# Kernel tuning notes

Measured on AMD Instinct MI355X. Metric: run time of the kernel, lower is better.

The kernel has to match this reference:

```python
import jax, jax.numpy as jnp
import numpy as np

H = 356  # CHAR_EMBED_DIM (100) + ELMO_EMBED_DIM (256)
CHAR_VOCAB = 96
CHAR_DIM = 100
N_FILT = 100
KW = 5
N_CTX = 8192
N_Q = 1024
W_CHARS = 16


def setup_inputs() -> dict:
    key = jax.random.key(0)
    ks = iter(jax.random.split(key, 32))
    s = 0.05
    inp = {}
    inp['ctx_char_ids'] = jax.random.randint(next(ks), (N_CTX, W_CHARS), 0, CHAR_VOCAB, dtype=jnp.int32)
    inp['q_char_ids'] = jax.random.randint(next(ks), (N_Q, W_CHARS), 0, CHAR_VOCAB, dtype=jnp.int32)
    inp['ctx_elmo'] = jax.random.normal(next(ks), (N_CTX, 256), jnp.float32)
    inp['q_elmo'] = jax.random.normal(next(ks), (N_Q, 256), jnp.float32)
    inp['char_emb'] = jax.random.normal(next(ks), (CHAR_VOCAB, CHAR_DIM), jnp.float32)
    inp['conv_w'] = jax.random.normal(next(ks), (N_FILT, CHAR_DIM, KW), jnp.float32) * s
    inp['conv_b'] = jax.random.normal(next(ks), (N_FILT,), jnp.float32) * s
    # Highway: 2 layers of plain + gate Linear(356 -> 356)
    inp['hw_pw'] = jax.random.normal(next(ks), (2, H, H), jnp.float32) * s
    inp['hw_pb'] = jax.random.normal(next(ks), (2, H), jnp.float32) * s
    inp['hw_gw'] = jax.random.normal(next(ks), (2, H, H), jnp.float32) * s
    inp['hw_gb'] = jax.random.normal(next(ks), (2, H), jnp.float32) * s
    # BiLSTM layer 0: input 356; layer 1: input 712. dims: [dir, 4H, Din]
    inp['w_ih0'] = jax.random.normal(next(ks), (2, 4 * H, H), jnp.float32) * s
    inp['w_hh0'] = jax.random.normal(next(ks), (2, 4 * H, H), jnp.float32) * s
    inp['b_ih0'] = jax.random.normal(next(ks), (2, 4 * H), jnp.float32) * s
    inp['b_hh0'] = jax.random.normal(next(ks), (2, 4 * H), jnp.float32) * s
    inp['w_ih1'] = jax.random.normal(next(ks), (2, 4 * H, 2 * H), jnp.float32) * s
    inp['w_hh1'] = jax.random.normal(next(ks), (2, 4 * H, H), jnp.float32) * s
    inp['b_ih1'] = jax.random.normal(next(ks), (2, 4 * H), jnp.float32) * s
    inp['b_hh1'] = jax.random.normal(next(ks), (2, 4 * H), jnp.float32) * s
    # randomize_init_hidden=True: random (h0, c0), shared per original code.
    h0 = jax.random.normal(next(ks), (2, 2, H), jnp.float32)  # [layer, dir, H]
    inp['h0'] = h0
    inp['c0'] = h0  # original returns (init_hidden, init_hidden)
    return inp


def _highway(x, pw, pb, gw, gb):
    for i in range(2):
        g = jax.nn.sigmoid(x @ gw[i].T + gb[i])
        p = jax.nn.relu(x @ pw[i].T + pb[i])
        x = g * p + (1.0 - g) * x
    return x


def _lstm_dir(x, w_ih, w_hh, b_ih, b_hh, h0, c0):
    # x: [T, Din]; PyTorch gate order i, f, g, o
    xg = x @ w_ih.T + (b_ih + b_hh)  # [T, 4H]

    def step(carry, xg_t):
        h, c = carry
        gates = xg_t + h @ w_hh.T
        i, f, g, o = jnp.split(gates, 4)
        i = jax.nn.sigmoid(i)
        f = jax.nn.sigmoid(f)
        g = jnp.tanh(g)
        o = jax.nn.sigmoid(o)
        c = f * c + i * g
        h = o * jnp.tanh(c)
        return (h, c), h

    _, hs = jax.lax.scan(step, (h0, c0), xg)
    return hs  # [T, H]


def _bilstm_layer(x, w_ih, w_hh, b_ih, b_hh, h0, c0):
    fwd = _lstm_dir(x, w_ih[0], w_hh[0], b_ih[0], b_hh[0], h0[0], c0[0])
    bwd = _lstm_dir(x[::-1], w_ih[1], w_hh[1], b_ih[1], b_hh[1], h0[1], c0[1])[::-1]
    return jnp.concatenate([fwd, bwd], axis=-1)  # [T, 2H]


def _embed_doc(char_ids, elmo, char_emb, conv_w, conv_b, hw_pw, hw_pb, hw_gw, hw_gb,
               w_ih0, w_hh0, b_ih0, b_hh0, w_ih1, w_hh1, b_ih1, b_hh1, h0, c0):
    ce = char_emb[char_ids]                  # [N, W, 100]
    x = jnp.transpose(ce, (0, 2, 1))         # [N, 100, W]
    conv = jax.lax.conv_general_dilated(
        x, conv_w, window_strides=(1,), padding=[(KW // 2, KW // 2)],
        dimension_numbers=('NCH', 'OIH', 'NCH')) + conv_b[None, :, None]
    cnn_feat = conv.max(axis=2)              # [N, 100] maxpool over char positions
    feats = jnp.concatenate([cnn_feat, elmo], axis=1)  # [N, 356]
    hwy = _highway(feats, hw_pw, hw_pb, hw_gw, hw_gb)
    l1 = _bilstm_layer(hwy, w_ih0, w_hh0, b_ih0, b_hh0, h0[0], c0[0])
    l2 = _bilstm_layer(l1, w_ih1, w_hh1, b_ih1, b_hh1, h0[1], c0[1])
    return l2  # [N, 712]


def reference(ctx_char_ids, q_char_ids, ctx_elmo, q_elmo, char_emb, conv_w, conv_b,
              hw_pw, hw_pb, hw_gw, hw_gb,
              w_ih0, w_hh0, b_ih0, b_hh0, w_ih1, w_hh1, b_ih1, b_hh1, h0, c0):
    params = (char_emb, conv_w, conv_b, hw_pw, hw_pb, hw_gw, hw_gb,
              w_ih0, w_hh0, b_ih0, b_hh0, w_ih1, w_hh1, b_ih1, b_hh1, h0, c0)
    ctx_out = _embed_doc(ctx_char_ids, ctx_elmo, *params)
    q_out = _embed_doc(q_char_ids, q_elmo, *params)
    return (ctx_out, q_out)
```

## Files before the change

kernel.cpp:

```cpp
#include <hip/hip_runtime.h>
#include <hip/hip_bf16.h>

#define H_DIM 356
#define G4 1424
#define NCTX 8192
#define NQ 1024
#define NTOT 9216
#define CDIM 100
#define NFILT 100
#define KW 5
#define WCH 16

typedef _Float16 f16_t;

__device__ __forceinline__ float sigmoidf_fast(float x) {
    return 1.0f / (1.0f + __expf(-x));
}
__device__ __forceinline__ float tanhf_fast(float x) {
    return 2.0f / (1.0f + __expf(-2.0f * x)) - 1.0f;
}
__device__ __forceinline__ unsigned pack_f16x2(float a, float b) {
    _Float16 ha = (_Float16)a, hb = (_Float16)b;
    unsigned short ua = __builtin_bit_cast(unsigned short, ha);
    unsigned short ub = __builtin_bit_cast(unsigned short, hb);
    return (unsigned)ua | ((unsigned)ub << 16);
}
__device__ __forceinline__ unsigned short f16_bits(float a) {
    _Float16 ha = (_Float16)a;
    return __builtin_bit_cast(unsigned short, ha);
}

#define FDOT_S(ACC, W, HS) \
    asm("v_dot2_f32_f16 %0, %1, %2, %0" : "+v"(ACC) : "v"(W), "s"(HS))

__global__ __launch_bounds__(128) void cnn_highway_kernel(
    const int* __restrict__ ctx_ids, const int* __restrict__ q_ids,
    const float* __restrict__ ctx_elmo, const float* __restrict__ q_elmo,
    const float* __restrict__ char_emb, const float* __restrict__ conv_w,
    const float* __restrict__ conv_b,
    const float* __restrict__ hw_pw, const float* __restrict__ hw_pb,
    const float* __restrict__ hw_gw, const float* __restrict__ hw_gb,
    float* __restrict__ feats_out)
{
    __shared__ float s_ce[WCH][CDIM];
    __shared__ float s_feats[16][H_DIM];
    const int tid  = threadIdx.x;
    const int row0 = blockIdx.x * 16;

    for (int rr = 0; rr < 16; ++rr) {
        const int row = row0 + rr;
        const int* ids = (row < NCTX) ? (ctx_ids + (size_t)row * WCH)
                                      : (q_ids + (size_t)(row - NCTX) * WCH);
        for (int idx = tid; idx < WCH * CDIM; idx += 128) {
            int w = idx / CDIM, c = idx - w * CDIM;
            s_ce[w][c] = char_emb[(size_t)ids[w] * CDIM + c];
        }
        __syncthreads();
        if (tid < NFILT) {
            const int f = tid;
            float s[WCH];
            float bias = conv_b[f];
            #pragma unroll
            for (int p = 0; p < WCH; ++p) s[p] = bias;
            const float* wrow = conv_w + (size_t)f * CDIM * KW;
            for (int c0 = 0; c0 < CDIM; c0 += 4) {
                float wv[20];
                const float4* wp4 = (const float4*)(wrow + c0 * KW);
                #pragma unroll
                for (int u = 0; u < 5; ++u) {
                    float4 v = wp4[u];
                    wv[u * 4 + 0] = v.x; wv[u * 4 + 1] = v.y;
                    wv[u * 4 + 2] = v.z; wv[u * 4 + 3] = v.w;
                }
                #pragma unroll
                for (int cc = 0; cc < 4; ++cc) {
                    float ce[WCH];
                    #pragma unroll
                    for (int w = 0; w < WCH; ++w) ce[w] = s_ce[w][c0 + cc];
                    #pragma unroll
                    for (int p = 0; p < WCH; ++p) {
                        #pragma unroll
                        for (int k = 0; k < KW; ++k) {
                            const int wpos = p + k - 2;
                            if (wpos >= 0 && wpos < WCH)
                                s[p] = fmaf(ce[wpos], wv[cc * 5 + k], s[p]);
                        }
                    }
                }
            }
            float m = s[0];
            #pragma unroll
            for (int p = 1; p < WCH; ++p) m = fmaxf(m, s[p]);
            s_feats[rr][f] = m;
        }
        __syncthreads();
    }

    for (int idx = tid; idx < 16 * 256; idx += 128) {
        int rr = idx >> 8, c = idx & 255;
        int row = row0 + rr;
        float v = (row < NCTX) ? ctx_elmo[(size_t)row * 256 + c]
                               : q_elmo[(size_t)(row - NCTX) * 256 + c];
        s_feats[rr][CDIM + c] = v;
    }
    __syncthreads();

    for (int l = 0; l < 2; ++l) {
        float newv[3][16];
        for (int it = 0; it < 3; ++it) {
            const int j = it * 128 + tid;
            if (j < H_DIM) {
                float accP[16], accG[16];
                #pragma unroll
                for (int r = 0; r < 16; ++r) { accP[r] = 0.0f; accG[r] = 0.0f; }
                const float* pw = hw_pw + ((size_t)l * H_DIM + j) * H_DIM;
                const float* gw = hw_gw + ((size_t)l * H_DIM + j) * H_DIM;
                for (int k0 = 0; k0 < H_DIM; k0 += 4) {
                    float4 wpv4 = *(const float4*)(pw + k0);
                    float4 wgv4 = *(const float4*)(gw + k0);
                    float wp[4] = {wpv4.x, wpv4.y, wpv4.z, wpv4.w};
                    float wg[4] = {wgv4.x, wgv4.y, wgv4.z, wgv4.w};
                    #pragma unroll
                    for (int kk = 0; kk < 4; ++kk) {
                        #pragma unroll
                        for (int r = 0; r < 16; ++r) {
                            float fv = s_feats[r][k0 + kk];
                            accP[r] = fmaf(fv, wp[kk], accP[r]);
                            accG[r] = fmaf(fv, wg[kk], accG[r]);
                        }
                    }
                }
                const float pb = hw_pb[l * H_DIM + j];
                const float gb = hw_gb[l * H_DIM + j];
                #pragma unroll
                for (int r = 0; r < 16; ++r) {
                    float p = accP[r] + pb; p = p > 0.0f ? p : 0.0f;
                    float g = sigmoidf_fast(accG[r] + gb);
                    newv[it][r] = g * p + (1.0f - g) * s_feats[r][j];
                }
            }
        }
        __syncthreads();
        for (int it = 0; it < 3; ++it) {
            const int j = it * 128 + tid;
            if (j < H_DIM) {
                #pragma unroll
                for (int r = 0; r < 16; ++r) s_feats[r][j] = newv[it][r];
            }
        }
        __syncthreads();
    }

    for (int idx = tid; idx < 16 * H_DIM; idx += 128) {
        int rr = idx / H_DIM, j = idx - rr * H_DIM;
        feats_out[(size_t)(row0 + rr) * H_DIM + j] = s_feats[rr][j];
    }
}

__global__ __launch_bounds__(256) void gemm_nt_bias_kernel(
    const float* __restrict__ A, const float* __restrict__ B,
    const float* __restrict__ bia, const float* __restrict__ bib,
    f16_t* __restrict__ C, int M, int N, int K)
{
    const int z = blockIdx.z;
    const float* Bz = B + (size_t)z * N * K;
    f16_t* Cz = C + (size_t)z * M * N;
    const int n0 = blockIdx.x * 64;
    const int m0 = blockIdx.y * 64;
    __shared__ float As[64][17];
    __shared__ float Bs[64][17];
    const int tid = threadIdx.x;
    const int tx = tid & 15, ty = tid >> 4;
    const int lr = tid >> 2;
    const int lc = (tid & 3) * 4;
    float acc[4][4];
    #pragma unroll
    for (int i = 0; i < 4; ++i)
        #pragma unroll
        for (int j = 0; j < 4; ++j) acc[i][j] = 0.0f;

    const int ktiles = (K + 15) / 16;
    for (int kt = 0; kt < ktiles; ++kt) {
        const int k0 = kt * 16;
        float4 av = {0, 0, 0, 0}, bv = {0, 0, 0, 0};
        if (k0 + lc < K)
            av = *(const float4*)(A + (size_t)(m0 + lr) * K + k0 + lc);
        const int bn = n0 + lr;
        if (bn < N && k0 + lc < K)
            bv = *(const float4*)(Bz + (size_t)bn * K + k0 + lc);
        __syncthreads();
        As[lr][lc + 0] = av.x; As[lr][lc + 1] = av.y;
        As[lr][lc + 2] = av.z; As[lr][lc + 3] = av.w;
        Bs[lr][lc + 0] = bv.x; Bs[lr][lc + 1] = bv.y;
        Bs[lr][lc + 2] = bv.z; Bs[lr][lc + 3] = bv.w;
        __syncthreads();
        #pragma unroll
        for (int kk = 0; kk < 16; ++kk) {
            float a[4], b[4];
            #pragma unroll
            for (int i = 0; i < 4; ++i) a[i] = As[ty * 4 + i][kk];
            #pragma unroll
            for (int j = 0; j < 4; ++j) b[j] = Bs[tx * 4 + j][kk];
            #pragma unroll
            for (int i = 0; i < 4; ++i)
                #pragma unroll
                for (int j = 0; j < 4; ++j)
                    acc[i][j] = fmaf(a[i], b[j], acc[i][j]);
        }
    }
    #pragma unroll
    for (int j = 0; j < 4; ++j) {
        const int n = n0 + tx * 4 + j;
        if (n < N) {
            const float bsum = bia[(size_t)z * N + n] + bib[(size_t)z * N + n];
            #pragma unroll
            for (int i = 0; i < 4; ++i) {
                const int m = m0 + ty * 4 + i;
                Cz[(size_t)m * N + n] = (f16_t)(acc[i][j] + bsum);
            }
        }
    }
}

__global__ __launch_bounds__(768)
__attribute__((amdgpu_waves_per_eu(3, 3)))
void lstm_scan_tag_kernel(
    const f16_t* __restrict__ xg,
    const float* __restrict__ whh,
    const float* __restrict__ h0,
    const float* __restrict__ c0,
    float* __restrict__ out,
    unsigned* hbuf,
    int tagbase)
{
    const int bid = blockIdx.x;
    const int s = bid & 7;
    if (s >= 4) return;
    const int sub = bid >> 3;
    const int doc = s >> 1, dir = s & 1;
    const int T = doc ? NQ : NCTX;
    const int rbase = doc ? NCTX : 0;
    const int soff = (s == 0) ? 0 : (s == 1) ? 8193 : (s == 2) ? 16386 : 17411;
    unsigned* hb = hbuf + (size_t)soff * 384;
    const int s0 = sub * 89;
    const int tid = threadIdx.x;
    const int lane = tid & 63;

    __shared__ float s_part[768];

    const int wv   = tid >> 6;
    const int half = (wv >= 6) ? 1 : 0;
    const int wi   = half ? (wv - 6) : wv;
    const int r    = wi * 64 + lane;
    const bool act = (r < 356);
    const int g = act ? (r / 89) : 0;
    const int j = act ? (r - 89 * g) : 0;
    const int rg = g * H_DIM + s0 + j;

    unsigned w[96];
    if (act) {
        const float* wrow = whh + ((size_t)dir * G4 + rg) * H_DIM;
        #pragma unroll
        for (int sl = 0; sl < 2; ++sl) {
            const int cb = 89 * (half * 2 + sl);
            #pragma unroll
            for (int p = 0; p < 44; ++p)
                w[48 * sl + p] = pack_f16x2(wrow[cb + 2 * p], wrow[cb + 2 * p + 1]);
            w[48 * sl + 44] = pack_f16x2(wrow[cb + 88], 0.0f);
            w[48 * sl + 45] = 0u; w[48 * sl + 46] = 0u; w[48 * sl + 47] = 0u;
        }
    } else {
        #pragma unroll
        for (int q = 0; q < 96; ++q) w[q] = 0u;
    }

    float c_state = 0.0f;
    if (tid < 96) {
        unsigned short hv = 0;
        if (tid < 89) {
            c_state = c0[dir * H_DIM + s0 + tid];
            hv = f16_bits(h0[dir * H_DIM + s0 + tid]);
        }
        __hip_atomic_store(&hb[sub * 96 + tid],
                           ((unsigned)(tagbase + 1) << 16) | hv,
                           __ATOMIC_RELAXED, __HIP_MEMORY_SCOPE_AGENT);
    }

    const f16_t* xgd = xg + (size_t)dir * NTOT * G4;

    for (int t = 0; t < T; ++t) {
        const int row = rbase + (dir ? (T - 1 - t) : t);
        float xv = 0.0f;
        if (!half && act) xv = (float)xgd[(size_t)row * G4 + rg];

        const unsigned want = (unsigned)(tagbase + t + 1);
        const unsigned* hw_ = hb + (size_t)t * 384 + half * 192;
        const int kb = (lane < 48) ? 4 * lane : 188;
        unsigned w0, w1, w2, w3;
        do {
            w0 = __hip_atomic_load(&hw_[kb],     __ATOMIC_RELAXED,
                                   __HIP_MEMORY_SCOPE_AGENT);
            w1 = __hip_atomic_load(&hw_[kb + 1], __ATOMIC_RELAXED,
                                   __HIP_MEMORY_SCOPE_AGENT);
            w2 = __hip_atomic_load(&hw_[kb + 2], __ATOMIC_RELAXED,
                                   __HIP_MEMORY_SCOPE_AGENT);
            w3 = __hip_atomic_load(&hw_[kb + 3], __ATOMIC_RELAXED,
                                   __HIP_MEMORY_SCOPE_AGENT);
        } while ((w0 >> 16) != want || (w1 >> 16) != want ||
                 (w2 >> 16) != want || (w3 >> 16) != want);
        const unsigned lo = (w0 & 0xffffu) | (w1 << 16);
        const unsigned hi = (w2 & 0xffffu) | (w3 << 16);

        float a0 = xv, a1 = 0.0f, a2 = 0.0f, a3 = 0.0f;
        #pragma unroll
        for (int q = 0; q < 96; q += 4) {
            const unsigned h0q = __builtin_amdgcn_readlane(lo, (q >> 1));
            const unsigned h1q = __builtin_amdgcn_readlane(hi, (q >> 1));
            const unsigned h2q = __builtin_amdgcn_readlane(lo, (q >> 1) + 1);
            const unsigned h3q = __builtin_amdgcn_readlane(hi, (q >> 1) + 1);
            FDOT_S(a0, w[q],     h0q);
            FDOT_S(a1, w[q + 1], h1q);
            FDOT_S(a2, w[q + 2], h2q);
            FDOT_S(a3, w[q + 3], h3q);
        }
        if (act) s_part[half * 384 + r] = (a0 + a1) + (a2 + a3);
        __syncthreads();

        if (tid < 96) {
            unsigned short hvbits = 0;
            if (tid < 89) {
                const float gi = s_part[tid]       + s_part[384 + tid];
                const float gf = s_part[89 + tid]  + s_part[384 + 89 + tid];
                const float gg = s_part[178 + tid] + s_part[384 + 178 + tid];
                const float go = s_part[267 + tid] + s_part[384 + 267 + tid];
                const float ii = sigmoidf_fast(gi);
                const float ff = sigmoidf_fast(gf);
                const float gt = tanhf_fast(gg);
                const float oo = sigmoidf_fast(go);
                c_state = ff * c_state + ii * gt;
                const float hh = oo * tanhf_fast(c_state);
                out[(size_t)row * 712 + dir * H_DIM + s0 + tid] = hh;
                hvbits = f16_bits(hh);
            }
            __hip_atomic_store(&hb[(size_t)(t + 1) * 384 + sub * 96 + tid],
                               ((unsigned)(tagbase + t + 2) << 16) | hvbits,
                               __ATOMIC_RELAXED, __HIP_MEMORY_SCOPE_AGENT);
        }
        __syncthreads();
    }
}

extern "C" void kernel_launch(void* const* d_in, const int* in_sizes, int n_in,
                              void* d_out, int out_size, void* d_ws, size_t ws_size,
                              hipStream_t stream) {
    (void)in_sizes; (void)n_in; (void)out_size; (void)ws_size;
    const int*   ctx_ids  = (const int*)d_in[0];
    const int*   q_ids    = (const int*)d_in[1];
    const float* ctx_elmo = (const float*)d_in[2];
    const float* q_elmo   = (const float*)d_in[3];
    const float* char_emb = (const float*)d_in[4];
    const float* conv_w   = (const float*)d_in[5];
    const float* conv_b   = (const float*)d_in[6];
    const float* hw_pw    = (const float*)d_in[7];
    const float* hw_pb    = (const float*)d_in[8];
    const float* hw_gw    = (const float*)d_in[9];
    const float* hw_gb    = (const float*)d_in[10];
    const float* w_ih0    = (const float*)d_in[11];
    const float* w_hh0    = (const float*)d_in[12];
    const float* b_ih0    = (const float*)d_in[13];
    const float* b_hh0    = (const float*)d_in[14];
    const float* w_ih1    = (const float*)d_in[15];
    const float* w_hh1    = (const float*)d_in[16];
    const float* b_ih1    = (const float*)d_in[17];
    const float* b_hh1    = (const float*)d_in[18];
    const float* h0       = (const float*)d_in[19];
    const float* c0       = (const float*)d_in[20];
    float* out = (float*)d_out;

    f16_t* xg    = (f16_t*)d_ws;
    float* feats = (float*)((char*)d_ws + (size_t)2 * NTOT * G4 * sizeof(f16_t));
    float* l1out = feats + (size_t)NTOT * H_DIM;
    unsigned* hbuf = (unsigned*)(l1out + (size_t)NTOT * 712);

    hipMemsetAsync(hbuf, 0, (size_t)18436 * 384 * sizeof(unsigned), stream);

    cnn_highway_kernel<<<NTOT / 16, 128, 0, stream>>>(
        ctx_ids, q_ids, ctx_elmo, q_elmo, char_emb, conv_w, conv_b,
        hw_pw, hw_pb, hw_gw, hw_gb, feats);

    dim3 ggrid((G4 + 63) / 64, NTOT / 64, 2);
    gemm_nt_bias_kernel<<<ggrid, 256, 0, stream>>>(
        feats, w_ih0, b_ih0, b_hh0, xg, NTOT, G4, H_DIM);

    lstm_scan_tag_kernel<<<32, 768, 0, stream>>>(
        xg, w_hh0, h0, c0, l1out, hbuf, 0);

    gemm_nt_bias_kernel<<<ggrid, 256, 0, stream>>>(
        l1out, w_ih1, b_ih1, b_hh1, xg, NTOT, G4, 2 * H_DIM);

    lstm_scan_tag_kernel<<<32, 768, 0, stream>>>(
        xg, w_hh1, h0 + 2 * H_DIM, c0 + 2 * H_DIM, out, hbuf, 16384);
}
```

Before: 35.35 ms.

## Split LSTM recurrence across 8 blocks per sequence instead of 4

Each sequence-direction's hidden state is now partitioned over 8 workgroups (44-45 units each) rather than 4 (89 units), with each block's 12 waves split into 4 K-quarters of the recurrent matvec. Per-thread weight registers halve and per-step dot-product work per block halves, aiming to shorten the serial per-timestep critical path. In exchange, more blocks must poll and publish through the global tagged h buffer each step, raising cross-block synchronisation traffic, and the shared-memory reduction grows to 4 partial sums.

```diff
diff --git a/kernel.cpp b/kernel.cpp
--- a/kernel.cpp
+++ b/kernel.cpp
@@ -224,7 +224,7 @@
 
 __global__ __launch_bounds__(768)
 __attribute__((amdgpu_waves_per_eu(3, 3)))
-void lstm_scan_tag_kernel(
+void lstm_scan8_kernel(
     const f16_t* __restrict__ xg,
     const float* __restrict__ whh,
     const float* __restrict__ h0,
@@ -242,47 +242,54 @@
     const int rbase = doc ? NCTX : 0;
     const int soff = (s == 0) ? 0 : (s == 1) ? 8193 : (s == 2) ? 16386 : 17411;
     unsigned* hb = hbuf + (size_t)soff * 384;
-    const int s0 = sub * 89;
+    const int cnt = (sub < 4) ? 45 : 44;
+    const int os  = 44 * sub + (sub < 4 ? sub : 4);
     const int tid = threadIdx.x;
     const int lane = tid & 63;
 
-    __shared__ float s_part[768];
-
-    const int wv   = tid >> 6;
-    const int half = (wv >= 6) ? 1 : 0;
-    const int wi   = half ? (wv - 6) : wv;
-    const int r    = wi * 64 + lane;
-    const bool act = (r < 356);
-    const int g = act ? (r / 89) : 0;
-    const int j = act ? (r - 89 * g) : 0;
-    const int rg = g * H_DIM + s0 + j;
-
-    unsigned w[96];
+    __shared__ float s_part[4][192];
+
+    const int wvi = tid >> 6;
+    const int qd  = wvi & 3;
+    const int rgp = wvi >> 2;
+    const int r   = rgp * 64 + lane;
+    const bool act = (r < 4 * cnt);
+    const int gate = act ? (r / cnt) : 0;
+    const int off  = act ? (r - gate * cnt) : 0;
+    const int grow = gate * H_DIM + os + off;
+
+    unsigned w[48];
     if (act) {
-        const float* wrow = whh + ((size_t)dir * G4 + rg) * H_DIM;
+        const float* wrow = whh + ((size_t)dir * G4 + grow) * H_DIM + 89 * qd;
         #pragma unroll
-        for (int sl = 0; sl < 2; ++sl) {
-            const int cb = 89 * (half * 2 + sl);
-            #pragma unroll
-            for (int p = 0; p < 44; ++p)
-                w[48 * sl + p] = pack_f16x2(wrow[cb + 2 * p], wrow[cb + 2 * p + 1]);
-            w[48 * sl + 44] = pack_f16x2(wrow[cb + 88], 0.0f);
-            w[48 * sl + 45] = 0u; w[48 * sl + 46] = 0u; w[48 * sl + 47] = 0u;
-        }
+        for (int p = 0; p < 44; ++p)
+            w[p] = pack_f16x2(wrow[2 * p], wrow[2 * p + 1]);
+        w[44] = pack_f16x2(wrow[88], 0.0f);
+        w[45] = 0u; w[46] = 0u; w[47] = 0u;
     } else {
         #pragma unroll
-        for (int q = 0; q < 96; ++q) w[q] = 0u;
+        for (int p = 0; p < 48; ++p) w[p] = 0u;
+    }
+
+    const int npub = cnt + (sub < 4 ? 7 : 0);
+    int pubw = 0;
+    if (tid < npub) {
+        if (tid < cnt) {
+            const int i = os + tid;
+            pubw = 96 * (i / 89) + (i % 89);
+        } else {
+            pubw = 96 * sub + 89 + (tid - cnt);
+        }
     }
 
     float c_state = 0.0f;
-    if (tid < 96) {
+    if (tid < npub) {
         unsigned short hv = 0;
-        if (tid < 89) {
-            c_state = c0[dir * H_DIM + s0 + tid];
-            hv = f16_bits(h0[dir * H_DIM + s0 + tid]);
-        }
-        __hip_atomic_store(&hb[sub * 96 + tid],
-                           ((unsigned)(tagbase + 1) << 16) | hv,
+        if (tid < cnt) {
+            c_state = c0[dir * H_DIM + os + tid];
+            hv = f16_bits(h0[dir * H_DIM + os + tid]);
+        }
+        __hip_atomic_store(&hb[pubw], ((unsigned)(tagbase + 1) << 16) | hv,
                            __ATOMIC_RELAXED, __HIP_MEMORY_SCOPE_AGENT);
     }
 
@@ -291,11 +298,11 @@
     for (int t = 0; t < T; ++t) {
         const int row = rbase + (dir ? (T - 1 - t) : t);
         float xv = 0.0f;
-        if (!half && act) xv = (float)xgd[(size_t)row * G4 + rg];
+        if (qd == 0 && act) xv = (float)xgd[(size_t)row * G4 + grow];
 
         const unsigned want = (unsigned)(tagbase + t + 1);
-        const unsigned* hw_ = hb + (size_t)t * 384 + half * 192;
-        const int kb = (lane < 48) ? 4 * lane : 188;
+        const unsigned* hw_ = hb + (size_t)t * 384 + 96 * qd;
+        const int kb = (lane < 24) ? 4 * lane : 92;
         unsigned w0, w1, w2, w3;
         do {
             w0 = __hip_atomic_load(&hw_[kb],     __ATOMIC_RELAXED,
@@ -308,41 +315,45 @@
                                    __HIP_MEMORY_SCOPE_AGENT);
         } while ((w0 >> 16) != want || (w1 >> 16) != want ||
                  (w2 >> 16) != want || (w3 >> 16) != want);
-        const unsigned lo = (w0 & 0xffffu) | (w1 << 16);
-        const unsigned hi = (w2 & 0xffffu) | (w3 << 16);
+        const unsigned p0 = (w0 & 0xffffu) | (w1 << 16);
+        const unsigned p1 = (w2 & 0xffffu) | (w3 << 16);
 
         float a0 = xv, a1 = 0.0f, a2 = 0.0f, a3 = 0.0f;
         #pragma unroll
-        for (int q = 0; q < 96; q += 4) {
-            const unsigned h0q = __builtin_amdgcn_readlane(lo, (q >> 1));
-            const unsigned h1q = __builtin_amdgcn_readlane(hi, (q >> 1));
-            const unsigned h2q = __builtin_amdgcn_readlane(lo, (q >> 1) + 1);
-            const unsigned h3q = __builtin_amdgcn_readlane(hi, (q >> 1) + 1);
+        for (int q = 0; q < 48; q += 4) {
+            const unsigned h0q = __builtin_amdgcn_readlane(p0, (q >> 1));
+            const unsigned h1q = __builtin_amdgcn_readlane(p1, (q >> 1));
+            const unsigned h2q = __builtin_amdgcn_readlane(p0, (q >> 1) + 1);
+            const unsigned h3q = __builtin_amdgcn_readlane(p1, (q >> 1) + 1);
             FDOT_S(a0, w[q],     h0q);
             FDOT_S(a1, w[q + 1], h1q);
             FDOT_S(a2, w[q + 2], h2q);
             FDOT_S(a3, w[q + 3], h3q);
         }
-        if (act) s_part[half * 384 + r] = (a0 + a1) + (a2 + a3);
-        __syncthreads();
-
-        if (tid < 96) {
+        if (act) s_part[qd][r] = (a0 + a1) + (a2 + a3);
+        __syncthreads();
+
+        if (tid < npub) {
             unsigned short hvbits = 0;
-            if (tid < 89) {
-                const float gi = s_part[tid]       + s_part[384 + tid];
-                const float gf = s_part[89 + tid]  + s_part[384 + 89 + tid];
-                const float gg = s_part[178 + tid] + s_part[384 + 178 + tid];
-                const float go = s_part[267 + tid] + s_part[384 + 267 + tid];
+            if (tid < cnt) {
+                const float gi = s_part[0][tid] + s_part[1][tid]
+                               + s_part[2][tid] + s_part[3][tid];
+                const float gf = s_part[0][cnt + tid] + s_part[1][cnt + tid]
+                               + s_part[2][cnt + tid] + s_part[3][cnt + tid];
+                const float gg = s_part[0][2*cnt + tid] + s_part[1][2*cnt + tid]
+                               + s_part[2][2*cnt + tid] + s_part[3][2*cnt + tid];
+                const float go = s_part[0][3*cnt + tid] + s_part[1][3*cnt + tid]
+                               + s_part[2][3*cnt + tid] + s_part[3][3*cnt + tid];
                 const float ii = sigmoidf_fast(gi);
                 const float ff = sigmoidf_fast(gf);
                 const float gt = tanhf_fast(gg);
                 const float oo = sigmoidf_fast(go);
                 c_state = ff * c_state + ii * gt;
                 const float hh = oo * tanhf_fast(c_state);
-                out[(size_t)row * 712 + dir * H_DIM + s0 + tid] = hh;
+                out[(size_t)row * 712 + dir * H_DIM + os + tid] = hh;
                 hvbits = f16_bits(hh);
             }
-            __hip_atomic_store(&hb[(size_t)(t + 1) * 384 + sub * 96 + tid],
+            __hip_atomic_store(&hb[(size_t)(t + 1) * 384 + pubw],
                                ((unsigned)(tagbase + t + 2) << 16) | hvbits,
                                __ATOMIC_RELAXED, __HIP_MEMORY_SCOPE_AGENT);
         }
@@ -392,12 +403,12 @@
     gemm_nt_bias_kernel<<<ggrid, 256, 0, stream>>>(
         feats, w_ih0, b_ih0, b_hh0, xg, NTOT, G4, H_DIM);
 
-    lstm_scan_tag_kernel<<<32, 768, 0, stream>>>(
+    lstm_scan8_kernel<<<64, 768, 0, stream>>>(
         xg, w_hh0, h0, c0, l1out, hbuf, 0);
 
     gemm_nt_bias_kernel<<<ggrid, 256, 0, stream>>>(
         l1out, w_ih1, b_ih1, b_hh1, xg, NTOT, G4, 2 * H_DIM);
 
-    lstm_scan_tag_kernel<<<32, 768, 0, stream>>>(
+    lstm_scan8_kernel<<<64, 768, 0, stream>>>(
         xg, w_hh1, h0 + 2 * H_DIM, c0 + 2 * H_DIM, out, hbuf, 16384);
 }
```

Measured after the change: 32.42 ms. -8.3%, faster.
